# Optimization experiments

Hardware: AMD Instinct MI355X
Metric: run time of the kernel (lower is better)

## Reference

```python
import jax, jax.numpy as jnp
import numpy as np

N = 200_000          # nodes (chain graph)
E = N - 1            # edges = diff structure
F = 5                # node features: [pos, vel_hist(3), cur_vel]
L = 16               # latent_size
G = 2                # globals: [time, static_param]
D = 3 * L + G        # ODE state dim = node_lat + sent_agg + recv_agg + globals
NSTEPS = 4           # fixed RK4 steps standing in for adaptive Tsit5 over t in [0,1]
DT = 0.01            # integrator dt of the physics post-processor


def setup_inputs() -> dict:
    key = jax.random.key(0)
    ks = iter(jax.random.split(key, 32))
    s = 0.1  # small init so the ODE stays well-behaved
    p = lambda shape: jax.random.normal(next(ks), shape, jnp.float32) * s
    inp = {}
    inp["nodes"] = jax.random.normal(next(ks), (N, F), jnp.float32)
    inp["edges"] = jax.random.normal(next(ks), (E, 1), jnp.float32)
    inp["g"] = jnp.zeros((G,), jnp.float32)
    inp["enc_n_w1"] = p((F, L)); inp["enc_n_b1"] = jnp.zeros((L,), jnp.float32)
    inp["enc_n_w2"] = p((L, L)); inp["enc_n_b2"] = jnp.zeros((L,), jnp.float32)
    inp["enc_e_w1"] = p((1, L)); inp["enc_e_b1"] = jnp.zeros((L,), jnp.float32)
    inp["enc_e_w2"] = p((L, L)); inp["enc_e_b2"] = jnp.zeros((L,), jnp.float32)
    inp["ode_w1"] = p((D + 1, D)); inp["ode_b1"] = jnp.zeros((D,), jnp.float32)
    inp["ode_w2"] = p((D, D)); inp["ode_b2"] = jnp.zeros((D,), jnp.float32)
    inp["node_out_w"] = p((D, L)); inp["node_out_b"] = jnp.zeros((L,), jnp.float32)
    inp["dec_n_w1"] = p((L, L)); inp["dec_n_b1"] = jnp.zeros((L,), jnp.float32)
    inp["dec_n_w2"] = p((L, L)); inp["dec_n_b2"] = jnp.zeros((L,), jnp.float32)
    inp["dec_n_w3"] = p((L, 1)); inp["dec_n_b3"] = jnp.zeros((1,), jnp.float32)
    inp["senders"] = jnp.arange(E, dtype=jnp.int32)
    inp["receivers"] = jnp.arange(1, N, dtype=jnp.int32)
    return inp


def reference(nodes, edges, g,
              enc_n_w1, enc_n_b1, enc_n_w2, enc_n_b2,
              enc_e_w1, enc_e_b1, enc_e_w2, enc_e_b2,
              ode_w1, ode_b1, ode_w2, ode_b2,
              node_out_w, node_out_b,
              dec_n_w1, dec_n_b1, dec_n_w2, dec_n_b2, dec_n_w3, dec_n_b3,
              senders, receivers):
    swish = jax.nn.swish
    n = nodes.shape[0]
    cur_pos = nodes[:, 0]
    cur_vel = nodes[:, -1]

    # --- encoder: MLP [L, L] on nodes and edges (swish, no final act) ---
    nlat = swish(nodes @ enc_n_w1 + enc_n_b1) @ enc_n_w2 + enc_n_b2   # [N, L]
    elat = swish(edges @ enc_e_w1 + enc_e_b1) @ enc_e_w2 + enc_e_b2   # [E, L]

    # --- processor (1 MP step): gather/scatter + Neural-ODE node update ---
    sent = jax.ops.segment_sum(elat, senders, num_segments=n)        # [N, L]
    recv = jax.ops.segment_sum(elat, receivers, num_segments=n)      # [N, L]
    gb = jnp.broadcast_to(g, (n, g.shape[0]))                        # [N, G]
    y0 = jnp.concatenate([nlat, sent, recv, gb], axis=1)             # [N, D]

    def f(t, y):  # derivative net: relu MLP on concat(y, t)
        inp = jnp.concatenate([y, jnp.full((y.shape[0], 1), t, y.dtype)], axis=1)
        return jax.nn.relu(inp @ ode_w1 + ode_b1) @ ode_w2 + ode_b2

    h = jnp.float32(1.0 / NSTEPS)

    def step(carry, _):
        y, t = carry
        k1 = f(t, y)
        k2 = f(t + 0.5 * h, y + 0.5 * h * k1)
        k3 = f(t + 0.5 * h, y + 0.5 * h * k2)
        k4 = f(t + h, y + h * k3)
        y = y + (h / 6.0) * (k1 + 2.0 * k2 + 2.0 * k3 + k4)
        return (y, t + h), None

    (yT, _), _ = jax.lax.scan(step, (y0, jnp.float32(0.0)), None, length=NSTEPS)
    nlat2 = yT @ node_out_w + node_out_b                             # [N, L]

    # --- global update: increment time ---
    g_new = jnp.concatenate([g[:1] + 1.0, g[1:]])

    # --- decoder node MLP [L, L, 1] ---
    dh = swish(nlat2 @ dec_n_w1 + dec_n_b1)
    dh = swish(dh @ dec_n_w2 + dec_n_b2)
    pred_acc = (dh @ dec_n_w3 + dec_n_b3).reshape(-1)                # [N]

    # --- semi-implicit Euler post-processor ---
    next_vel = cur_vel + pred_acc * DT
    next_pos = cur_pos + next_vel * DT
    next_nodes = jnp.column_stack([next_pos, nodes[:, 2:], next_vel, pred_acc])
    next_edges = jnp.diff(next_pos).reshape(-1, 1)
    return next_nodes, next_edges, g_new
```

## Files before the change

kernel.cpp:

```cpp
#include <hip/hip_runtime.h>

#define NN 200000
#define EE (NN - 1)
#define NSTEPS 4
#define DTC 0.01f
#define WPB 4
#define NPB 128
#define GRID 1563

typedef __attribute__((ext_vector_type(8))) _Float16 f16x8;
typedef __attribute__((ext_vector_type(2))) _Float16 f16x2;
typedef __attribute__((ext_vector_type(4))) float f32x4;

struct H4 { f16x2 a, b, c, d; };

__device__ __forceinline__ f16x2 c2h(float lo, float hi) {
    return __builtin_bit_cast(f16x2, __builtin_amdgcn_cvt_pkrtz(lo, hi));
}
__device__ __forceinline__ unsigned pk2h(float lo, float hi) {
    return __builtin_bit_cast(unsigned, __builtin_amdgcn_cvt_pkrtz(lo, hi));
}
__device__ __forceinline__ f16x8 h8(f16x2 a, f16x2 b, f16x2 c, f16x2 d) {
    H4 t{a, b, c, d};
    return __builtin_bit_cast(f16x8, t);
}
__device__ __forceinline__ f16x2 relu2(f16x2 v) {
    f16x2 r;
    asm("v_pk_max_f16 %0, %1, 0" : "=v"(r) : "v"(v));
    return r;
}
__device__ __forceinline__ float swishf(float x) { return x / (1.0f + __expf(-x)); }

__device__ __forceinline__ int permk(int k) {
    return (k & 0x23) | ((k & 4) << 2) | ((k & 0x18) >> 1);
}

__device__ __forceinline__ f16x8 setw(f16x8 v, bool cond, unsigned nw) {
    uint4 u = __builtin_bit_cast(uint4, v);
    u.w = cond ? nw : u.w;
    return __builtin_bit_cast(f16x8, u);
}

__global__ void gnode_weights(const float* __restrict__ ode_w1, const float* __restrict__ ode_b1,
                              const float* __restrict__ ode_w2, const float* __restrict__ ode_b2,
                              const float* __restrict__ enc_n_w2, const float* __restrict__ enc_e_w2,
                              const float* __restrict__ dec_n_w1, const float* __restrict__ dec_n_w2,
                              const float* __restrict__ node_out_w,
                              unsigned short* __restrict__ wg)
{
    const int b = blockIdx.x;
    const int tid = threadIdx.x;
    if (b < 8) {
        const int i = tid + b * 256;
        const int od = i >> 5;
        const int k2 = (i & 31) * 2;
        const int s0 = permk(k2);
        const int s1 = s0 + 1;
        float a0 = 0.f, a1 = 0.f, b0 = 0.f, b1 = 0.f;
        if (od < 50) {
            a0 = (s0 <= 50) ? ode_w1[s0 * 50 + od] : 0.f;
            a1 = (s1 <= 50) ? ode_w1[s1 * 50 + od]
                            : ((s1 == 51) ? ode_b1[od] : 0.f);
            b0 = (s0 < 50) ? ode_w2[s0 * 50 + od]
                           : ((s0 == 50) ? ode_b2[od] : 0.f);
            b1 = (s1 < 50) ? ode_w2[s1 * 50 + od] : 0.f;
        }
        *(unsigned*)(wg + od * 64 + k2) = pk2h(a0, a1);
        *(unsigned*)(wg + 4096 + od * 64 + k2) = pk2h(b0, b1);
    } else if (b < 10) {
        const int i = tid + (b - 8) * 256;
        const int mm = i >> 5;
        const int kp = (i & 31) * 2;
        const int s0 = permk(kp);
        const float v0 = (s0     < 50) ? node_out_w[s0 * 16 + mm] : 0.f;
        const float v1 = (s0 + 1 < 50) ? node_out_w[(s0 + 1) * 16 + mm] : 0.f;
        *(unsigned*)(wg + 10240 + mm * 64 + kp) = pk2h(v0, v1);
    } else {
        const int mm = tid >> 4;
        const int kp = (tid & 15) * 2;
        const bool rl = (kp < 16);
        const float eN0 = rl ? enc_n_w2[kp * 16 + mm] : 0.f;
        const float eN1 = rl ? enc_n_w2[(kp + 1) * 16 + mm] : 0.f;
        const float eE0 = rl ? enc_e_w2[kp * 16 + mm] : 0.f;
        const float eE1 = rl ? enc_e_w2[(kp + 1) * 16 + mm] : 0.f;
        const float d10 = rl ? dec_n_w1[kp * 16 + mm] : 0.f;
        const float d11 = rl ? dec_n_w1[(kp + 1) * 16 + mm] : 0.f;
        const float d20 = rl ? dec_n_w2[kp * 16 + mm] : 0.f;
        const float d21 = rl ? dec_n_w2[(kp + 1) * 16 + mm] : 0.f;
        *(unsigned*)(wg + 8192 + mm * 32 + kp) = pk2h(eN0, eN1);
        *(unsigned*)(wg + 8704 + mm * 32 + kp) = pk2h(eE0, eE1);
        *(unsigned*)(wg + 9216 + mm * 32 + kp) = pk2h(d10, d11);
        *(unsigned*)(wg + 9728 + mm * 32 + kp) = pk2h(d20, d21);
    }
}

__global__ __launch_bounds__(256, 3)
void gnode_main(const float* __restrict__ nodes,
                const float* __restrict__ edges,
                const float* __restrict__ g,
                const float* __restrict__ enc_n_w1, const float* __restrict__ enc_n_b1,
                const float* __restrict__ enc_n_b2,
                const float* __restrict__ enc_e_w1, const float* __restrict__ enc_e_b1,
                const float* __restrict__ enc_e_b2,
                const float* __restrict__ node_out_b,
                const float* __restrict__ dec_n_b1, const float* __restrict__ dec_n_b2,
                const float* __restrict__ dec_n_w3, const float* __restrict__ dec_n_b3,
                const unsigned short* __restrict__ wg,
                float* __restrict__ out, float* __restrict__ npos)
{
    __shared__ __attribute__((aligned(16))) unsigned short dscr[WPB][640];

    const int tid  = threadIdx.x;
    const int lane = tid & 63;
    const int wave = __builtin_amdgcn_readfirstlane(tid >> 6);
    const int m = lane & 15;
    const int q = lane >> 4;
    const bool q0 = (q == 0);
    unsigned short* const dscrw = &dscr[wave][0];

    int nd[2], nc[2];
    nd[0] = blockIdx.x * NPB + wave * 32 + m;
    nd[1] = nd[0] + 16;
    nc[0] = (nd[0] < NN) ? nd[0] : (NN - 1);
    nc[1] = (nd[1] < NN) ? nd[1] : (NN - 1);

    *(uint2*)(dscrw + m * 40 + 16 + q * 4) = make_uint2(0u, 0u);

    f16x8 w1f[2][4], w2f[2][4];
#pragma unroll
    for (int kt = 0; kt < 2; ++kt)
#pragma unroll
        for (int ct = 0; ct < 4; ++ct) {
            const int od = ct * 16 + m;
            w1f[kt][ct] = *(const f16x8*)(const void*)(wg + od * 64 + kt * 32 + q * 8);
            w2f[kt][ct] = *(const f16x8*)(const void*)(wg + 4096 + od * 64 + kt * 32 + q * 8);
        }

    const f32x4 zero4 = {0.f, 0.f, 0.f, 0.f};
    const f16x2 h2z = {(_Float16)0.f, (_Float16)0.f};
    const f16x8 z8 = h8(h2z, h2z, h2z, h2z);

    f16x8 Y[2][2], ACC[2][2], A[2][2];

    {
        const f16x8 wNf = *(const f16x8*)(const void*)(wg + 8192 + m * 32 + q * 8);
        const f16x8 wEf = *(const f16x8*)(const void*)(wg + 8704 + m * 32 + q * 8);
        f32x4 bN, bE;
#pragma unroll
        for (int r = 0; r < 4; ++r) { bN[r] = enc_n_b2[q * 4 + r]; bE[r] = enc_e_b2[q * 4 + r]; }
        const float g0v = g[0], g1v = g[1];

#pragma unroll
        for (int tt = 0; tt < 2; ++tt) {
            const int node = nc[tt];
            f32x4 e0, e1, e2;
            {
                float nf[5];
#pragma unroll
                for (int c = 0; c < 5; ++c) nf[c] = nodes[node * 5 + c];
                f16x8 bfr = z8;
                if (q < 2) {
                    float hv[8];
#pragma unroll
                    for (int j = 0; j < 8; ++j) {
                        const int d = q * 8 + j;
                        float s = enc_n_b1[d];
#pragma unroll
                        for (int c = 0; c < 5; ++c) s = fmaf(nf[c], enc_n_w1[c * 16 + d], s);
                        hv[j] = swishf(s);
                    }
                    bfr = h8(c2h(hv[0], hv[1]), c2h(hv[2], hv[3]),
                             c2h(hv[4], hv[5]), c2h(hv[6], hv[7]));
                }
                e0 = __builtin_amdgcn_mfma_f32_16x16x32_f16(wNf, bfr, bN, 0, 0, 0);
            }
            {
                const float ev = (node < EE) ? edges[node] : 0.0f;
                f16x8 bfr = z8;
                if (q < 2) {
                    float hv[8];
#pragma unroll
                    for (int j = 0; j < 8; ++j) {
                        const int d = q * 8 + j;
                        hv[j] = swishf(fmaf(ev, enc_e_w1[d], enc_e_b1[d]));
                    }
                    bfr = h8(c2h(hv[0], hv[1]), c2h(hv[2], hv[3]),
                             c2h(hv[4], hv[5]), c2h(hv[6], hv[7]));
                }
                e1 = __builtin_amdgcn_mfma_f32_16x16x32_f16(wEf, bfr, bE, 0, 0, 0);
                if (node == NN - 1) e1 = zero4;
            }
            {
                const float ev = (node > 0) ? edges[node - 1] : 0.0f;
                f16x8 bfr = z8;
                if (q < 2) {
                    float hv[8];
#pragma unroll
                    for (int j = 0; j < 8; ++j) {
                        const int d = q * 8 + j;
                        hv[j] = swishf(fmaf(ev, enc_e_w1[d], enc_e_b1[d]));
                    }
                    bfr = h8(c2h(hv[0], hv[1]), c2h(hv[2], hv[3]),
                             c2h(hv[4], hv[5]), c2h(hv[6], hv[7]));
                }
                e2 = __builtin_amdgcn_mfma_f32_16x16x32_f16(wEf, bfr, bE, 0, 0, 0);
                if (node == 0) e2 = zero4;
            }
            Y[tt][0] = h8(c2h(e0[0], e0[1]), c2h(e0[2], e0[3]),
                          c2h(e1[0], e1[1]), c2h(e1[2], e1[3]));
            Y[tt][1] = h8(c2h(e2[0], e2[1]), c2h(e2[2], e2[3]),
                          q0 ? c2h(g0v, g1v) : h2z, h2z);
            A[tt][0] = Y[tt][0];
            A[tt][1] = setw(Y[tt][1], q0, pk2h(0.f, 1.f));
        }
    }

    const float hh = 1.0f / NSTEPS;
    float t0 = 0.0f;
    const unsigned one2 = 0x3C003C00u;

#pragma clang loop unroll(disable)
    for (int stage = 0; stage < 4 * NSTEPS; ++stage) {
        const int s = stage & 3;

        f32x4 hc[2][4];
#pragma unroll
        for (int ct = 0; ct < 4; ++ct) {
            f32x4 c0 = __builtin_amdgcn_mfma_f32_16x16x32_f16(w1f[0][ct], A[0][0], zero4, 0, 0, 0);
            f32x4 c1 = __builtin_amdgcn_mfma_f32_16x16x32_f16(w1f[0][ct], A[1][0], zero4, 0, 0, 0);
            hc[0][ct] = __builtin_amdgcn_mfma_f32_16x16x32_f16(w1f[1][ct], A[0][1], c0, 0, 0, 0);
            hc[1][ct] = __builtin_amdgcn_mfma_f32_16x16x32_f16(w1f[1][ct], A[1][1], c1, 0, 0, 0);
        }
        f16x8 H[2][2];
#pragma unroll
        for (int tt = 0; tt < 2; ++tt) {
            H[tt][0] = h8(relu2(c2h(hc[tt][0][0], hc[tt][0][1])),
                          relu2(c2h(hc[tt][0][2], hc[tt][0][3])),
                          relu2(c2h(hc[tt][1][0], hc[tt][1][1])),
                          relu2(c2h(hc[tt][1][2], hc[tt][1][3])));
            f16x8 h1 = h8(relu2(c2h(hc[tt][2][0], hc[tt][2][1])),
                          relu2(c2h(hc[tt][2][2], hc[tt][2][3])),
                          relu2(c2h(hc[tt][3][0], hc[tt][3][1])),
                          relu2(c2h(hc[tt][3][2], hc[tt][3][3])));
            H[tt][1] = setw(h1, q0, one2);
        }
        f32x4 kc[2][4];
#pragma unroll
        for (int ct = 0; ct < 4; ++ct) {
            f32x4 c0 = __builtin_amdgcn_mfma_f32_16x16x32_f16(w2f[0][ct], H[0][0], zero4, 0, 0, 0);
            f32x4 c1 = __builtin_amdgcn_mfma_f32_16x16x32_f16(w2f[0][ct], H[1][0], zero4, 0, 0, 0);
            kc[0][ct] = __builtin_amdgcn_mfma_f32_16x16x32_f16(w2f[1][ct], H[0][1], c0, 0, 0, 0);
            kc[1][ct] = __builtin_amdgcn_mfma_f32_16x16x32_f16(w2f[1][ct], H[1][1], c1, 0, 0, 0);
        }

        const float ca = (s == 0 || s == 3) ? hh / 6.0f : hh / 3.0f;
        const float cb = (s == 2) ? hh : 0.5f * hh;
        const f16x2 cah = c2h(ca, ca);
        const f16x2 cbh = c2h(cb, cb);
        const f16x8 ca8 = h8(cah, cah, cah, cah);
        const f16x8 cb8 = h8(cbh, cbh, cbh, cbh);
        float tn;
        if (s < 3) tn = t0 + cb;
        else { t0 += hh; tn = t0; }
        const unsigned tw = pk2h(tn, 1.0f);

#pragma unroll
        for (int tt = 0; tt < 2; ++tt) {
            f16x8 KC0 = h8(c2h(kc[tt][0][0], kc[tt][0][1]), c2h(kc[tt][0][2], kc[tt][0][3]),
                           c2h(kc[tt][1][0], kc[tt][1][1]), c2h(kc[tt][1][2], kc[tt][1][3]));
            f16x8 KC1 = h8(c2h(kc[tt][2][0], kc[tt][2][1]), c2h(kc[tt][2][2], kc[tt][2][3]),
                           c2h(kc[tt][3][0], kc[tt][3][1]), c2h(kc[tt][3][2], kc[tt][3][3]));
            if (s == 0) {
                ACC[tt][0] = ca8 * KC0 + Y[tt][0];
                ACC[tt][1] = ca8 * KC1 + Y[tt][1];
            } else {
                ACC[tt][0] = ca8 * KC0 + ACC[tt][0];
                ACC[tt][1] = ca8 * KC1 + ACC[tt][1];
            }
            f16x8 av0, av1;
            if (s < 3) {
                av0 = cb8 * KC0 + Y[tt][0];
                av1 = cb8 * KC1 + Y[tt][1];
            } else {
                Y[tt][0] = ACC[tt][0];
                Y[tt][1] = ACC[tt][1];
                av0 = ACC[tt][0];
                av1 = ACC[tt][1];
            }
            A[tt][0] = av0;
            A[tt][1] = setw(av1, q0, tw);
        }
    }

    const f16x8 dw1 = *(const f16x8*)(const void*)(wg + 9216 + m * 32 + q * 8);
    const f16x8 dw2 = *(const f16x8*)(const void*)(wg + 9728 + m * 32 + q * 8);
    const f16x8 ow0 = *(const f16x8*)(const void*)(wg + 10240 + m * 64 + q * 8);
    const f16x8 ow1 = *(const f16x8*)(const void*)(wg + 10240 + m * 64 + 32 + q * 8);
    f32x4 bO, bD1, bD2;
    float w3v[4];
#pragma unroll
    for (int r = 0; r < 4; ++r) {
        bO[r]  = node_out_b[q * 4 + r];
        bD1[r] = dec_n_b1[q * 4 + r];
        bD2[r] = dec_n_b2[q * 4 + r];
        w3v[r] = dec_n_w3[q * 4 + r];
    }

#pragma unroll
    for (int tt = 0; tt < 2; ++tt) {
        f32x4 nl2 = __builtin_amdgcn_mfma_f32_16x16x32_f16(ow0, Y[tt][0], bO, 0, 0, 0);
        nl2       = __builtin_amdgcn_mfma_f32_16x16x32_f16(ow1, Y[tt][1], nl2, 0, 0, 0);

        *(uint2*)(dscrw + m * 40 + q * 4) =
            make_uint2(pk2h(nl2[0], nl2[1]), pk2h(nl2[2], nl2[3]));
        f16x8 nB = *(const f16x8*)(const void*)(dscrw + m * 40 + q * 8);
        f32x4 dh = __builtin_amdgcn_mfma_f32_16x16x32_f16(dw1, nB, bD1, 0, 0, 0);
#pragma unroll
        for (int r = 0; r < 4; ++r) dh[r] = swishf(dh[r]);

        *(uint2*)(dscrw + m * 40 + q * 4) =
            make_uint2(pk2h(dh[0], dh[1]), pk2h(dh[2], dh[3]));
        f16x8 dB = *(const f16x8*)(const void*)(dscrw + m * 40 + q * 8);
        f32x4 dh2 = __builtin_amdgcn_mfma_f32_16x16x32_f16(dw2, dB, bD2, 0, 0, 0);
#pragma unroll
        for (int r = 0; r < 4; ++r) dh2[r] = swishf(dh2[r]);

        float p = dh2[0] * w3v[0];
        p = fmaf(dh2[1], w3v[1], p);
        p = fmaf(dh2[2], w3v[2], p);
        p = fmaf(dh2[3], w3v[3], p);
        p += __shfl_xor(p, 16);
        p += __shfl_xor(p, 32);
        p += dec_n_b3[0];

        const int node = nd[tt];
        if (q0 && node < NN) {
            const float cur_pos = nodes[node * 5 + 0];
            const float c2 = nodes[node * 5 + 2];
            const float c3 = nodes[node * 5 + 3];
            const float cur_vel = nodes[node * 5 + 4];
            const float next_vel = fmaf(p, DTC, cur_vel);
            const float next_pos = fmaf(next_vel, DTC, cur_pos);
            out[node * 6 + 0] = next_pos;
            out[node * 6 + 1] = c2;
            out[node * 6 + 2] = c3;
            out[node * 6 + 3] = cur_vel;
            out[node * 6 + 4] = next_vel;
            out[node * 6 + 5] = p;
            npos[node] = next_pos;
        }
    }
}

__global__ void gnode_edges(const float* __restrict__ npos,
                            float* __restrict__ out,
                            const float* __restrict__ g)
{
    const int e = blockIdx.x * blockDim.x + threadIdx.x;
    if (e < EE) {
        out[NN * 6 + e] = npos[e + 1] - npos[e];
    }
    if (e == 0) {
        out[NN * 6 + EE]     = g[0] + 1.0f;
        out[NN * 6 + EE + 1] = g[1];
    }
}

extern "C" void kernel_launch(void* const* d_in, const int* in_sizes, int n_in,
                              void* d_out, int out_size, void* d_ws, size_t ws_size,
                              hipStream_t stream) {
    const float* nodes      = (const float*)d_in[0];
    const float* edges      = (const float*)d_in[1];
    const float* g          = (const float*)d_in[2];
    const float* enc_n_w1   = (const float*)d_in[3];
    const float* enc_n_b1   = (const float*)d_in[4];
    const float* enc_n_w2   = (const float*)d_in[5];
    const float* enc_n_b2   = (const float*)d_in[6];
    const float* enc_e_w1   = (const float*)d_in[7];
    const float* enc_e_b1   = (const float*)d_in[8];
    const float* enc_e_w2   = (const float*)d_in[9];
    const float* enc_e_b2   = (const float*)d_in[10];
    const float* ode_w1     = (const float*)d_in[11];
    const float* ode_b1     = (const float*)d_in[12];
    const float* ode_w2     = (const float*)d_in[13];
    const float* ode_b2     = (const float*)d_in[14];
    const float* node_out_w = (const float*)d_in[15];
    const float* node_out_b = (const float*)d_in[16];
    const float* dec_n_w1   = (const float*)d_in[17];
    const float* dec_n_b1   = (const float*)d_in[18];
    const float* dec_n_w2   = (const float*)d_in[19];
    const float* dec_n_b2   = (const float*)d_in[20];
    const float* dec_n_w3   = (const float*)d_in[21];
    const float* dec_n_b3   = (const float*)d_in[22];
    float* out  = (float*)d_out;
    float* npos = (float*)d_ws;
    unsigned short* wg = (unsigned short*)((char*)d_ws + (size_t)NN * 4);

    gnode_weights<<<11, 256, 0, stream>>>(
        ode_w1, ode_b1, ode_w2, ode_b2,
        enc_n_w2, enc_e_w2, dec_n_w1, dec_n_w2, node_out_w, wg);

    gnode_main<<<GRID, 256, 0, stream>>>(
        nodes, edges, g,
        enc_n_w1, enc_n_b1, enc_n_b2,
        enc_e_w1, enc_e_b1, enc_e_b2,
        node_out_b, dec_n_b1, dec_n_b2, dec_n_w3, dec_n_b3,
        wg, out, npos);

    gnode_edges<<<(EE + 255) / 256, 256, 0, stream>>>(npos, out, g);
}
```

Before: 176.6 us.

## Stage ODE MLP weights in shared memory instead of holding them in registers

The ODE weight matrices used to be held as 16 f16x8 register fragments per thread for the whole RK4 loop. They are now copied cooperatively into a 16 KB shared-memory array, stored in the prep kernel in a swizzled fragment order so each lane reads a contiguous 16-byte chunk, and reloaded from LDS before every MFMA group. This frees a large block of VGPRs, which could allow more waves per CU or reduce spilling. The cost is extra LDS traffic on every stage, a block-wide barrier, and more shared memory per block, which may itself limit occupancy.

New measurement: 172.0 us. -2.6%, faster.

```diff
diff --git a/kernel.cpp b/kernel.cpp
--- a/kernel.cpp
+++ b/kernel.cpp
@@ -65,8 +65,14 @@
                            : ((s0 == 50) ? ode_b2[od] : 0.f);
             b1 = (s1 < 50) ? ode_w2[s1 * 50 + od] : 0.f;
         }
-        *(unsigned*)(wg + od * 64 + k2) = pk2h(a0, a1);
-        *(unsigned*)(wg + 4096 + od * 64 + k2) = pk2h(b0, b1);
+        const int ct = od >> 4;
+        const int mm = od & 15;
+        const int kt = k2 >> 5;
+        const int qq = (k2 >> 3) & 3;
+        const int jj = k2 & 7;
+        const int didx = ct * 1024 + kt * 512 + (mm * 4 + qq) * 8 + jj;
+        *(unsigned*)(wg + didx) = pk2h(a0, a1);
+        *(unsigned*)(wg + 4096 + didx) = pk2h(b0, b1);
     } else if (b < 10) {
         const int i = tid + (b - 8) * 256;
         const int mm = i >> 5;
@@ -109,6 +115,7 @@
                 float* __restrict__ out, float* __restrict__ npos)
 {
     __shared__ __attribute__((aligned(16))) unsigned short dscr[WPB][640];
+    __shared__ __attribute__((aligned(16))) unsigned short sw[8192];
 
     const int tid  = threadIdx.x;
     const int lane = tid & 63;
@@ -118,6 +125,10 @@
     const bool q0 = (q == 0);
     unsigned short* const dscrw = &dscr[wave][0];
 
+#pragma unroll
+    for (int i = 0; i < 4; ++i)
+        ((uint4*)sw)[tid + 256 * i] = ((const uint4*)wg)[tid + 256 * i];
+
     int nd[2], nc[2];
     nd[0] = blockIdx.x * NPB + wave * 32 + m;
     nd[1] = nd[0] + 16;
@@ -125,16 +136,6 @@
     nc[1] = (nd[1] < NN) ? nd[1] : (NN - 1);
 
     *(uint2*)(dscrw + m * 40 + 16 + q * 4) = make_uint2(0u, 0u);
-
-    f16x8 w1f[2][4], w2f[2][4];
-#pragma unroll
-    for (int kt = 0; kt < 2; ++kt)
-#pragma unroll
-        for (int ct = 0; ct < 4; ++ct) {
-            const int od = ct * 16 + m;
-            w1f[kt][ct] = *(const f16x8*)(const void*)(wg + od * 64 + kt * 32 + q * 8);
-            w2f[kt][ct] = *(const f16x8*)(const void*)(wg + 4096 + od * 64 + kt * 32 + q * 8);
-        }
 
     const f32x4 zero4 = {0.f, 0.f, 0.f, 0.f};
     const f16x2 h2z = {(_Float16)0.f, (_Float16)0.f};
@@ -215,6 +216,10 @@
         }
     }
 
+    __syncthreads();
+
+    const unsigned short* const swl = sw + (m * 4 + q) * 8;
+
     const float hh = 1.0f / NSTEPS;
     float t0 = 0.0f;
     const unsigned one2 = 0x3C003C00u;
@@ -226,10 +231,12 @@
         f32x4 hc[2][4];
 #pragma unroll
         for (int ct = 0; ct < 4; ++ct) {
-            f32x4 c0 = __builtin_amdgcn_mfma_f32_16x16x32_f16(w1f[0][ct], A[0][0], zero4, 0, 0, 0);
-            f32x4 c1 = __builtin_amdgcn_mfma_f32_16x16x32_f16(w1f[0][ct], A[1][0], zero4, 0, 0, 0);
-            hc[0][ct] = __builtin_amdgcn_mfma_f32_16x16x32_f16(w1f[1][ct], A[0][1], c0, 0, 0, 0);
-            hc[1][ct] = __builtin_amdgcn_mfma_f32_16x16x32_f16(w1f[1][ct], A[1][1], c1, 0, 0, 0);
+            const f16x8 wa = *(const f16x8*)(const void*)(swl + ct * 1024);
+            const f16x8 wb = *(const f16x8*)(const void*)(swl + ct * 1024 + 512);
+            f32x4 c0 = __builtin_amdgcn_mfma_f32_16x16x32_f16(wa, A[0][0], zero4, 0, 0, 0);
+            f32x4 c1 = __builtin_amdgcn_mfma_f32_16x16x32_f16(wa, A[1][0], zero4, 0, 0, 0);
+            hc[0][ct] = __builtin_amdgcn_mfma_f32_16x16x32_f16(wb, A[0][1], c0, 0, 0, 0);
+            hc[1][ct] = __builtin_amdgcn_mfma_f32_16x16x32_f16(wb, A[1][1], c1, 0, 0, 0);
         }
         f16x8 H[2][2];
 #pragma unroll
@@ -247,10 +254,12 @@
         f32x4 kc[2][4];
 #pragma unroll
         for (int ct = 0; ct < 4; ++ct) {
-            f32x4 c0 = __builtin_amdgcn_mfma_f32_16x16x32_f16(w2f[0][ct], H[0][0], zero4, 0, 0, 0);
-            f32x4 c1 = __builtin_amdgcn_mfma_f32_16x16x32_f16(w2f[0][ct], H[1][0], zero4, 0, 0, 0);
-            kc[0][ct] = __builtin_amdgcn_mfma_f32_16x16x32_f16(w2f[1][ct], H[0][1], c0, 0, 0, 0);
-            kc[1][ct] = __builtin_amdgcn_mfma_f32_16x16x32_f16(w2f[1][ct], H[1][1], c1, 0, 0, 0);
+            const f16x8 wa = *(const f16x8*)(const void*)(swl + 4096 + ct * 1024);
+            const f16x8 wb = *(const f16x8*)(const void*)(swl + 4096 + ct * 1024 + 512);
+            f32x4 c0 = __builtin_amdgcn_mfma_f32_16x16x32_f16(wa, H[0][0], zero4, 0, 0, 0);
+            f32x4 c1 = __builtin_amdgcn_mfma_f32_16x16x32_f16(wa, H[1][0], zero4, 0, 0, 0);
+            kc[0][ct] = __builtin_amdgcn_mfma_f32_16x16x32_f16(wb, H[0][1], c0, 0, 0, 0);
+            kc[1][ct] = __builtin_amdgcn_mfma_f32_16x16x32_f16(wb, H[1][1], c1, 0, 0, 0);
         }
 
         const float ca = (s == 0 || s == 3) ? hh / 6.0f : hh / 3.0f;
```
